# Kernel tuning notes

Measured on AMD Instinct MI355X. Metric: run time of the kernel, lower is better.

## Reference

```python
import jax, jax.numpy as jnp
import numpy as np

B, S, T = 512, 512, 128


def setup_inputs() -> dict:
    key = jax.random.key(0)
    k1, k2, k3, k4, k5 = jax.random.split(key, 5)
    emissions = jax.random.normal(k1, (B, S, T), dtype=jnp.float32)
    tags = jax.random.randint(k2, (B, S), 0, T, dtype=jnp.int32)
    mask = jnp.ones((B, S), dtype=jnp.int32)
    start_transitions = jax.random.uniform(k3, (T,), minval=-0.1, maxval=0.1, dtype=jnp.float32)
    end_transitions = jax.random.uniform(k4, (T,), minval=-0.1, maxval=0.1, dtype=jnp.float32)
    transitions = jax.random.uniform(k5, (T, T), minval=-0.1, maxval=0.1, dtype=jnp.float32)
    return {"emissions": emissions, "tags": tags, "mask": mask,
            "start_transitions": start_transitions,
            "end_transitions": end_transitions,
            "transitions": transitions}


def reference(emissions, tags, mask, start_transitions, end_transitions, transitions):
    b, s, t = emissions.shape
    maskf = mask.astype(emissions.dtype)
    barange = jnp.arange(b)

    # ---- numerator: score of the gold path (vectorized over timesteps) ----
    score = start_transitions[tags[:, 0]] + emissions[barange, 0, tags[:, 0]]
    # transition scores tags[i-1] -> tags[i], shape (B, S-1)
    trans_steps = transitions[tags[:, :-1], tags[:, 1:]]
    # emission score of gold tag at each step, shape (B, S)
    em_steps = jnp.take_along_axis(emissions, tags[:, :, None], axis=2)[:, :, 0]
    score = score + jnp.sum((trans_steps + em_steps[:, 1:]) * maskf[:, 1:], axis=1)
    seq_ends = mask.astype(jnp.int32).sum(axis=1) - 1
    last_tags = tags[barange, seq_ends]
    score = score + end_transitions[last_tags]

    # ---- denominator: log partition via forward recurrence (lax.scan) ----
    init = start_transitions[None, :] + emissions[:, 0, :]  # (B, T)

    def step(scores, inp):
        em_i, m_i = inp  # (B, T), (B,)
        # (B, T_prev, T_next) semiring matmul in log-space
        nxt = jax.nn.logsumexp(
            scores[:, :, None] + transitions[None, :, :] + em_i[:, None, :], axis=1)
        scores = jnp.where(m_i[:, None] > 0, nxt, scores)
        return scores, None

    ems = jnp.moveaxis(emissions[:, 1:, :], 1, 0)  # (S-1, B, T)
    ms = jnp.moveaxis(mask[:, 1:], 1, 0)           # (S-1, B)
    final, _ = jax.lax.scan(step, init, (ems, ms))
    denom = jax.nn.logsumexp(final + end_transitions[None, :], axis=1)  # (B,)

    return jnp.sum(score - denom)
```

## Files before the change

kernel.cpp:

```cpp
#include <hip/hip_runtime.h>
#include <math.h>


#define T 128
#define SLEN 512
#define BATCH 512

typedef float v2f __attribute__((ext_vector_type(2)));

__global__ __launch_bounds__(256, 2) void fwd_kernel(
    const float* __restrict__ em, const int* __restrict__ tags,
    const int* __restrict__ mask, const float* __restrict__ startT,
    const float* __restrict__ endT, const float* __restrict__ trans,
    float* __restrict__ ws)
{
    const int tid = threadIdx.x;
    const int rg  = tid & 7;
    const int cg  = tid >> 3;
    const int q   = rg & 3;
    const int b   = blockIdx.x;
    const int jc  = 4 * cg + q;
    const float* emb = em + (size_t)b * SLEN * T;
    const int*   mk  = mask + (size_t)b * SLEN;

    int craw[4], slot[4];
#pragma unroll
    for (int i = 0; i < 4; ++i) {
        craw[i] = 4 * rg + ((i + rg) & 3);
        slot[i] = craw[i] ^ ((craw[i] & 16) ? 4 : 0);
    }

    v2f Elo[4][4], Ehi[4][4];
#pragma unroll
    for (int i = 0; i < 4; ++i) {
        const int r0 = 4 * craw[i];
#pragma unroll
        for (int qq = 0; qq < 4; ++qq) {
            const int col = 4 * cg + qq;
            Elo[i][qq] = (v2f){ __expf(trans[(r0 + 0) * T + col]),
                                __expf(trans[(r0 + 1) * T + col]) };
            Ehi[i][qq] = (v2f){ __expf(trans[(r0 + 2) * T + col]),
                                __expf(trans[(r0 + 3) * T + col]) };
        }
    }

    __shared__ __align__(16) float4 psh[2][32];
    __shared__ float reds[4], redn[4];
    __shared__ int   redc[4];

    const char* rp[4];
#pragma unroll
    for (int i = 0; i < 4; ++i)
        rp[i] = (const char*)&psh[0][0] + slot[i] * 16;
    const int scg = cg ^ ((cg & 16) ? 4 : 0);
    char* wp = (char*)&psh[0][0] + scg * 16 + q * 4;
    const char* srefp = (const char*)&psh[0][0];

    float pprev = __expf(startT[jc] + emb[jc]);
    if (rg < 4) *(float*)(wp + 512) = pprev;
    double Ld = 0.0;

    float emv[4], emn[4];
    int   mkv[4], mkn[4];
#pragma unroll
    for (int k = 0; k < 4; ++k) {
        emv[k] = __expf((emb + (1 + k) * T)[jc]);
        mkv[k] = mk[1 + k];
    }
    __syncthreads();

    const bool lb0 = (rg & 1) != 0, lb1 = (rg & 2) != 0;

    for (int s0 = 1; s0 < SLEN; s0 += 4) {
#pragma unroll
        for (int k = 0; k < 4; ++k) {
            int ss = s0 + 4 + k; ss = (ss < SLEN) ? ss : (SLEN - 1);
            emn[k] = (emb + ss * T)[jc];
            mkn[k] = mk[ss];
        }
#pragma unroll
        for (int k = 0; k < 4; ++k) {
            const int s = s0 + k;
            if (s < SLEN) {
                const int cur = (1 + k) & 1;
                const float sref0 = *(const float*)(srefp + cur * 512);
                const float srefc = fmaxf(sref0, 1e-30f);
                const float cc = __builtin_amdgcn_rcpf(srefc);
                const float f  = emv[k] * cc;
                Ld += (double)__logf(srefc);

                v2f a0 = {0.f, 0.f}, a1 = a0, a2 = a0, a3 = a0;
#pragma unroll
                for (int i = 0; i < 4; ++i) {
                    const float4 pv = *(const float4*)(rp[i] + cur * 512);
                    const v2f plo = {pv.x, pv.y}, phi = {pv.z, pv.w};
                    a0 = __builtin_elementwise_fma(plo, Elo[i][0], a0);
                    a0 = __builtin_elementwise_fma(phi, Ehi[i][0], a0);
                    a1 = __builtin_elementwise_fma(plo, Elo[i][1], a1);
                    a1 = __builtin_elementwise_fma(phi, Ehi[i][1], a1);
                    a2 = __builtin_elementwise_fma(plo, Elo[i][2], a2);
                    a2 = __builtin_elementwise_fma(phi, Ehi[i][2], a2);
                    a3 = __builtin_elementwise_fma(plo, Elo[i][3], a3);
                    a3 = __builtin_elementwise_fma(phi, Ehi[i][3], a3);
                }
                const float c0 = a0.x + a0.y, c1 = a1.x + a1.y;
                const float c2 = a2.x + a2.y, c3 = a3.x + a3.y;
                float P  = (lb0 ? c1 : c0) + __shfl_xor(lb0 ? c0 : c1, 1);
                float P2 = (lb0 ? c3 : c2) + __shfl_xor(lb0 ? c2 : c3, 1);
                float t  = (lb1 ? P2 : P) + __shfl_xor(lb1 ? P : P2, 2);
                t += __shfl_xor(t, 4);
                const float pn = t * f;
                const float pm = pprev * cc;
                pprev = (mkv[k] > 0) ? pn : pm;
                if (rg < 4) *(float*)(wp + (cur ^ 1) * 512) = pprev;
                __syncthreads();
            }
        }
#pragma unroll
        for (int k = 0; k < 4; ++k) { emv[k] = __expf(emn[k]); mkv[k] = mkn[k]; }
    }

    const int wid = tid >> 6;
    float sm = (rg < 4) ? pprev * __expf(endT[jc]) : 0.f;
#pragma unroll
    for (int off = 32; off; off >>= 1) sm += __shfl_xor(sm, off);
    if ((tid & 63) == 0) reds[wid] = sm;

    const int* tg = tags + (size_t)b * SLEN;
    float nv = 0.f; int cnt = 0;
#pragma unroll
    for (int rep = 0; rep < 2; ++rep) {
        const int s = tid + 256 * rep;
        const int mm = mk[s];
        cnt += (mm != 0);
        if (s >= 1 && mm > 0)
            nv += trans[tg[s - 1] * T + tg[s]] + emb[s * T + tg[s]];
    }
#pragma unroll
    for (int off = 32; off; off >>= 1) {
        nv  += __shfl_xor(nv, off);
        cnt += __shfl_xor(cnt, off);
    }
    if ((tid & 63) == 0) { redn[wid] = nv; redc[wid] = cnt; }
    __syncthreads();
    if (tid == 0) {
        float ssum = 0.f, nsum = 0.f; int seqlen = 0;
#pragma unroll
        for (int i = 0; i < 4; ++i) {
            ssum += reds[i]; nsum += redn[i]; seqlen += redc[i];
        }
        const float denom = __logf(ssum) + (float)Ld;
        const int t0 = tg[0], tl = tg[seqlen - 1];
        ws[b] = (startT[t0] + emb[t0] + endT[tl] + nsum) - denom;
    }
}

__global__ __launch_bounds__(256) void reduce_kernel(
    const float* __restrict__ ws, float* __restrict__ out)
{
    const int t = threadIdx.x;
    float local = 0.f;
    for (int i = t; i < BATCH; i += 256) local += ws[i];
    __shared__ float rf[256];
    rf[t] = local;
    __syncthreads();
    for (int off = 128; off > 0; off >>= 1) {
        if (t < off) rf[t] += rf[t + off];
        __syncthreads();
    }
    if (t == 0) out[0] = rf[0];
}

extern "C" void kernel_launch(void* const* d_in, const int* in_sizes, int n_in,
                              void* d_out, int out_size, void* d_ws, size_t ws_size,
                              hipStream_t stream)
{
    const float* emissions = (const float*)d_in[0];
    const int*   tags      = (const int*)d_in[1];
    const int*   mask      = (const int*)d_in[2];
    const float* startT    = (const float*)d_in[3];
    const float* endT      = (const float*)d_in[4];
    const float* trans     = (const float*)d_in[5];
    float* out = (float*)d_out;
    float* ws  = (float*)d_ws;

    fwd_kernel<<<BATCH, 256, 0, stream>>>(emissions, tags, mask, startT, endT, trans, ws);
    reduce_kernel<<<1, 256, 0, stream>>>(ws, out);
}
```

Measured before the change: 383.5 us.

## Run forward recurrence in a single wavefront per sequence without block barriers

Replaces the 256-thread block, which needed cross-lane shuffles and a __syncthreads every timestep, with one 64-lane wavefront per sequence. Each lane owns two output tags and keeps its full 128-row column of exp(transitions) in registers. The scaling reference is broadcast with readfirstlane, so neither the LDS read of it nor the barrier is needed. In exchange, each lane runs long dependent FMA chains per step and needs very high register pressure, with a risk of spills. Fewer waves per CU also leaves less latency hiding.

```diff
diff --git a/kernel.cpp b/kernel.cpp
--- a/kernel.cpp
+++ b/kernel.cpp
@@ -8,74 +8,60 @@
 
 typedef float v2f __attribute__((ext_vector_type(2)));
 
-__global__ __launch_bounds__(256, 2) void fwd_kernel(
+__device__ __forceinline__ float rdlane0(float x) {
+    return __int_as_float(__builtin_amdgcn_readfirstlane(__float_as_int(x)));
+}
+
+__global__ __launch_bounds__(64, 1)
+__attribute__((amdgpu_waves_per_eu(1, 1)))
+void fwd_kernel(
     const float* __restrict__ em, const int* __restrict__ tags,
     const int* __restrict__ mask, const float* __restrict__ startT,
     const float* __restrict__ endT, const float* __restrict__ trans,
     float* __restrict__ ws)
 {
-    const int tid = threadIdx.x;
-    const int rg  = tid & 7;
-    const int cg  = tid >> 3;
-    const int q   = rg & 3;
-    const int b   = blockIdx.x;
-    const int jc  = 4 * cg + q;
+    const int l  = threadIdx.x;
+    const int b  = blockIdx.x;
+    const int j0 = 2 * l, j1 = 2 * l + 1;
     const float* emb = em + (size_t)b * SLEN * T;
     const int*   mk  = mask + (size_t)b * SLEN;
 
-    int craw[4], slot[4];
+    v2f EA[64], EB[64];
 #pragma unroll
-    for (int i = 0; i < 4; ++i) {
-        craw[i] = 4 * rg + ((i + rg) & 3);
-        slot[i] = craw[i] ^ ((craw[i] & 16) ? 4 : 0);
+    for (int i = 0; i < 64; ++i) {
+        const float2 r0 = *(const float2*)(trans + (2 * i    ) * T + j0);
+        const float2 r1 = *(const float2*)(trans + (2 * i + 1) * T + j0);
+        EA[i] = (v2f){ __expf(r0.x), __expf(r1.x) };
+        EB[i] = (v2f){ __expf(r0.y), __expf(r1.y) };
     }
 
-    v2f Elo[4][4], Ehi[4][4];
-#pragma unroll
-    for (int i = 0; i < 4; ++i) {
-        const int r0 = 4 * craw[i];
-#pragma unroll
-        for (int qq = 0; qq < 4; ++qq) {
-            const int col = 4 * cg + qq;
-            Elo[i][qq] = (v2f){ __expf(trans[(r0 + 0) * T + col]),
-                                __expf(trans[(r0 + 1) * T + col]) };
-            Ehi[i][qq] = (v2f){ __expf(trans[(r0 + 2) * T + col]),
-                                __expf(trans[(r0 + 3) * T + col]) };
-        }
-    }
+    __shared__ __align__(16) float4 pbuf[2][T / 4];
 
-    __shared__ __align__(16) float4 psh[2][32];
-    __shared__ float reds[4], redn[4];
-    __shared__ int   redc[4];
+    char* wp = (char*)&pbuf[0][0] + 8 * l;
+    const float4* rb0 = &pbuf[0][0];
+    const float4* rb1 = &pbuf[1][0];
 
-    const char* rp[4];
-#pragma unroll
-    for (int i = 0; i < 4; ++i)
-        rp[i] = (const char*)&psh[0][0] + slot[i] * 16;
-    const int scg = cg ^ ((cg & 16) ? 4 : 0);
-    char* wp = (char*)&psh[0][0] + scg * 16 + q * 4;
-    const char* srefp = (const char*)&psh[0][0];
-
-    float pprev = __expf(startT[jc] + emb[jc]);
-    if (rg < 4) *(float*)(wp + 512) = pprev;
+    const float2 e0 = *(const float2*)(emb + j0);
+    v2f pprev = { __expf(startT[j0] + e0.x), __expf(startT[j1] + e0.y) };
+    *(v2f*)(wp + 512) = pprev;
+    float sref = rdlane0(pprev.x);
     double Ld = 0.0;
 
-    float emv[4], emn[4];
-    int   mkv[4], mkn[4];
+    v2f emv[4], emn[4];
+    int mkv[4], mkn[4];
 #pragma unroll
     for (int k = 0; k < 4; ++k) {
-        emv[k] = __expf((emb + (1 + k) * T)[jc]);
+        const float2 e = *(const float2*)(emb + (1 + k) * T + j0);
+        emv[k] = (v2f){ __expf(e.x), __expf(e.y) };
         mkv[k] = mk[1 + k];
     }
-    __syncthreads();
-
-    const bool lb0 = (rg & 1) != 0, lb1 = (rg & 2) != 0;
 
     for (int s0 = 1; s0 < SLEN; s0 += 4) {
 #pragma unroll
         for (int k = 0; k < 4; ++k) {
             int ss = s0 + 4 + k; ss = (ss < SLEN) ? ss : (SLEN - 1);
-            emn[k] = (emb + ss * T)[jc];
+            const float2 e = *(const float2*)(emb + ss * T + j0);
+            emn[k] = (v2f){ e.x, e.y };
             mkn[k] = mk[ss];
         }
 #pragma unroll
@@ -83,54 +69,46 @@
             const int s = s0 + k;
             if (s < SLEN) {
                 const int cur = (1 + k) & 1;
-                const float sref0 = *(const float*)(srefp + cur * 512);
-                const float srefc = fmaxf(sref0, 1e-30f);
+                const float4* rb = cur ? rb1 : rb0;
+                const float srefc = fmaxf(sref, 1e-30f);
                 const float cc = __builtin_amdgcn_rcpf(srefc);
-                const float f  = emv[k] * cc;
                 Ld += (double)__logf(srefc);
+                const v2f f2 = emv[k] * cc;
 
-                v2f a0 = {0.f, 0.f}, a1 = a0, a2 = a0, a3 = a0;
+                v2f accA = {0.f, 0.f}, accB = {0.f, 0.f};
 #pragma unroll
-                for (int i = 0; i < 4; ++i) {
-                    const float4 pv = *(const float4*)(rp[i] + cur * 512);
+                for (int i = 0; i < 32; ++i) {
+                    const float4 pv = rb[i];
                     const v2f plo = {pv.x, pv.y}, phi = {pv.z, pv.w};
-                    a0 = __builtin_elementwise_fma(plo, Elo[i][0], a0);
-                    a0 = __builtin_elementwise_fma(phi, Ehi[i][0], a0);
-                    a1 = __builtin_elementwise_fma(plo, Elo[i][1], a1);
-                    a1 = __builtin_elementwise_fma(phi, Ehi[i][1], a1);
-                    a2 = __builtin_elementwise_fma(plo, Elo[i][2], a2);
-                    a2 = __builtin_elementwise_fma(phi, Ehi[i][2], a2);
-                    a3 = __builtin_elementwise_fma(plo, Elo[i][3], a3);
-                    a3 = __builtin_elementwise_fma(phi, Ehi[i][3], a3);
+                    accA = __builtin_elementwise_fma(plo, EA[2 * i    ], accA);
+                    accA = __builtin_elementwise_fma(phi, EA[2 * i + 1], accA);
+                    accB = __builtin_elementwise_fma(plo, EB[2 * i    ], accB);
+                    accB = __builtin_elementwise_fma(phi, EB[2 * i + 1], accB);
                 }
-                const float c0 = a0.x + a0.y, c1 = a1.x + a1.y;
-                const float c2 = a2.x + a2.y, c3 = a3.x + a3.y;
-                float P  = (lb0 ? c1 : c0) + __shfl_xor(lb0 ? c0 : c1, 1);
-                float P2 = (lb0 ? c3 : c2) + __shfl_xor(lb0 ? c2 : c3, 1);
-                float t  = (lb1 ? P2 : P) + __shfl_xor(lb1 ? P : P2, 2);
-                t += __shfl_xor(t, 4);
-                const float pn = t * f;
-                const float pm = pprev * cc;
+                const v2f tt = { accA.x + accA.y, accB.x + accB.y };
+                const v2f pn = tt * f2;
+                const v2f pm = pprev * cc;
                 pprev = (mkv[k] > 0) ? pn : pm;
-                if (rg < 4) *(float*)(wp + (cur ^ 1) * 512) = pprev;
-                __syncthreads();
+                *(v2f*)(wp + (cur ^ 1) * 512) = pprev;
+                sref = rdlane0(pprev.x);
             }
         }
 #pragma unroll
-        for (int k = 0; k < 4; ++k) { emv[k] = __expf(emn[k]); mkv[k] = mkn[k]; }
+        for (int k = 0; k < 4; ++k) {
+            emv[k] = (v2f){ __expf(emn[k].x), __expf(emn[k].y) };
+            mkv[k] = mkn[k];
+        }
     }
 
-    const int wid = tid >> 6;
-    float sm = (rg < 4) ? pprev * __expf(endT[jc]) : 0.f;
+    float v = pprev.x * __expf(endT[j0]) + pprev.y * __expf(endT[j1]);
 #pragma unroll
-    for (int off = 32; off; off >>= 1) sm += __shfl_xor(sm, off);
-    if ((tid & 63) == 0) reds[wid] = sm;
+    for (int off = 32; off; off >>= 1) v += __shfl_xor(v, off);
 
     const int* tg = tags + (size_t)b * SLEN;
     float nv = 0.f; int cnt = 0;
 #pragma unroll
-    for (int rep = 0; rep < 2; ++rep) {
-        const int s = tid + 256 * rep;
+    for (int rep = 0; rep < 8; ++rep) {
+        const int s = l + 64 * rep;
         const int mm = mk[s];
         cnt += (mm != 0);
         if (s >= 1 && mm > 0)
@@ -141,17 +119,11 @@
         nv  += __shfl_xor(nv, off);
         cnt += __shfl_xor(cnt, off);
     }
-    if ((tid & 63) == 0) { redn[wid] = nv; redc[wid] = cnt; }
-    __syncthreads();
-    if (tid == 0) {
-        float ssum = 0.f, nsum = 0.f; int seqlen = 0;
-#pragma unroll
-        for (int i = 0; i < 4; ++i) {
-            ssum += reds[i]; nsum += redn[i]; seqlen += redc[i];
-        }
-        const float denom = __logf(ssum) + (float)Ld;
+    if (l == 0) {
+        const float denom = __logf(v) + (float)Ld;
+        const int seqlen = cnt;
         const int t0 = tg[0], tl = tg[seqlen - 1];
-        ws[b] = (startT[t0] + emb[t0] + endT[tl] + nsum) - denom;
+        ws[b] = (startT[t0] + emb[t0] + endT[tl] + nv) - denom;
     }
 }
 
@@ -184,6 +156,6 @@
     float* out = (float*)d_out;
     float* ws  = (float*)d_ws;
 
-    fwd_kernel<<<BATCH, 256, 0, stream>>>(emissions, tags, mask, startT, endT, trans, ws);
+    fwd_kernel<<<BATCH, 64, 0, stream>>>(emissions, tags, mask, startT, endT, trans, ws);
     reduce_kernel<<<1, 256, 0, stream>>>(ws, out);
 }
```

Measured after the change: 976.9 us. 2.55x slower.
